# Kernel optimization log

Measured on AMD Instinct MI355X. Metric: run time of the kernel, lower is better.

The kernel has to match this reference:

```python
import jax, jax.numpy as jnp
import numpy as np

B, T, C = 8, 512, 512
H, HKV, D = 8, 4, 64
S_MAX = 128
BASE_FREQ = 10000.0
INIT_SIGMA = 256.0
EPS = 1e-6


def _init_positional_kernel(n_heads, head_dim, s_max, base_freq):
    table_size = 2 * s_max + 1
    deltas = jnp.arange(table_size) - s_max
    d_half = head_dim // 2
    freqs = 1.0 / base_freq ** (jnp.arange(d_half, dtype=jnp.float32) / d_half)
    phases = deltas[:, None].astype(jnp.float32) * freqs[None, :]
    P_single = jnp.concatenate([jnp.cos(phases), jnp.sin(phases)], axis=-1)
    return jnp.tile(P_single[None, :, :], (n_heads, 1, 1))


def setup_inputs() -> dict:
    key = jax.random.key(0)
    ks = jax.random.split(key, 6)
    scale = 0.02
    x = jax.random.normal(ks[0], (B, T, C), dtype=jnp.float32)
    Wq = jax.random.normal(ks[1], (C, H * D), dtype=jnp.float32) * scale
    Wk = jax.random.normal(ks[2], (C, HKV * D), dtype=jnp.float32) * scale
    Wv = jax.random.normal(ks[3], (C, HKV * D), dtype=jnp.float32) * scale
    Wproj = jax.random.normal(ks[4], (C, C), dtype=jnp.float32) * scale
    P = _init_positional_kernel(H, D, S_MAX, BASE_FREQ)
    sigma = jnp.full((H,), INIT_SIGMA, dtype=jnp.float32)
    return {"x": x, "Wq": Wq, "Wk": Wk, "Wv": Wv, "Wproj": Wproj, "P": P, "sigma": sigma}


def _norm(t):
    # nGPT-style: unit norm * sqrt(dim)
    dim = t.shape[-1]
    return t * (jnp.sqrt(float(dim)) * jax.lax.rsqrt((t * t).sum(axis=-1, keepdims=True) + EPS))


def _warped_kernel(P, sigma, T_):
    # P: [H, 2*S_MAX+1, D], sigma: [H] -> P_interp: [H, T, T, D]
    positions = jnp.arange(T_)
    delta = positions[:, None] - positions[None, :]  # [T, T]
    s = jnp.abs(sigma) + 1e-6
    delta_warped = S_MAX * jnp.tanh(delta[None, :, :].astype(jnp.float32) / s[:, None, None])
    delta_table = delta_warped + S_MAX  # [H, T, T]
    idx_lo = jnp.floor(delta_table).astype(jnp.int32)
    idx_hi = idx_lo + 1
    frac = delta_table - idx_lo.astype(P.dtype)
    table_max = 2 * S_MAX
    idx_lo = jnp.clip(idx_lo, 0, table_max)
    idx_hi = jnp.clip(idx_hi, 0, table_max)
    head_idx = jnp.arange(H)[:, None, None]
    P_lo = P[head_idx, idx_lo, :]  # [H, T, T, D]
    P_hi = P[head_idx, idx_hi, :]
    return (1 - frac[..., None]) * P_lo + frac[..., None] * P_hi


def reference(x, Wq, Wk, Wv, Wproj, P, sigma):
    q = (x @ Wq).reshape(B, T, H, D)
    k = (x @ Wk).reshape(B, T, HKV, D)
    v = (x @ Wv).reshape(B, T, HKV, D)
    q, k = _norm(q), _norm(k)
    repeats = H // HKV
    k = jnp.repeat(k, repeats, axis=2)
    v = jnp.repeat(v, repeats, axis=2)
    q = q.transpose(0, 2, 1, 3)  # [B, H, T, D]
    k = k.transpose(0, 2, 1, 3)
    v = v.transpose(0, 2, 1, 3)

    sm_scale = 1.0 / jnp.sqrt(float(D))
    P_interp = _warped_kernel(P, sigma, T)  # [H, T, T, D]
    S = jnp.einsum('bhid,hijd,bhjd->bhij', q, P_interp, k) * sm_scale
    causal_mask = jnp.tril(jnp.ones((T, T), dtype=jnp.bool_))
    S = jnp.where(causal_mask[None, None, :, :], S, jnp.finfo(S.dtype).min)
    A = jax.nn.softmax(S, axis=-1)
    y = A @ v  # [B, H, T, D]
    y = y.transpose(0, 2, 1, 3).reshape(B, T, H * D)
    return y @ Wproj
```

## Files before the change

kernel.cpp:

```cpp
#include <hip/hip_runtime.h>
#include <hip/hip_bf16.h>
#include <math.h>

#define Bb 8
#define Tt 512
#define Cc 512
#define Hh 8
#define HKV 4
#define Dd 64

typedef __attribute__((ext_vector_type(8))) short short8;
typedef __attribute__((ext_vector_type(4))) float float4v;
typedef __attribute__((ext_vector_type(2))) __fp16 h2;

__device__ __forceinline__ h2 u2h(unsigned u) {
  union { unsigned u; h2 h; } x; x.u = u; return x.h;
}
__device__ __forceinline__ unsigned h2u(h2 h) {
  union { h2 h; unsigned u; } x; x.h = h; return x.u;
}
__device__ __forceinline__ float fdot2(h2 a, h2 b, float c) {
#if __has_builtin(__builtin_amdgcn_fdot2)
  return __builtin_amdgcn_fdot2(a, b, c, false);
#else
  return fmaf((float)a.x, (float)b.x, fmaf((float)a.y, (float)b.y, c));
#endif
}

__device__ __forceinline__ float wave_reduce_sum(float v) {
#pragma unroll
  for (int off = 32; off > 0; off >>= 1) v += __shfl_xor(v, off, 64);
  return v;
}
__device__ __forceinline__ unsigned pack_bf2(float a, float b) {
  __hip_bfloat162 h = __float22bfloat162_rn(make_float2(a, b));
  return *(unsigned*)&h;
}

__global__ __launch_bounds__(256) void conv_x(const float* __restrict__ x,
                                              unsigned short* __restrict__ xb) {
  int i = (blockIdx.x * 256 + threadIdx.x) * 8;
  float4 f0 = *(const float4*)&x[i];
  float4 f1 = *(const float4*)&x[i + 4];
  unsigned u[4] = {pack_bf2(f0.x, f0.y), pack_bf2(f0.z, f0.w),
                   pack_bf2(f1.x, f1.y), pack_bf2(f1.z, f1.w)};
  *(uint4*)&xb[i] = *(uint4*)u;
}

__global__ __launch_bounds__(256) void conv_w(
    const float* __restrict__ Wq, const float* __restrict__ Wk,
    const float* __restrict__ Wv, const float* __restrict__ Wp,
    unsigned short* __restrict__ Wtq, unsigned short* __restrict__ Wtp) {
  __shared__ float Ts[64][65];
  const int k0 = blockIdx.x * 64;
  const int n0 = blockIdx.y * 64;
  const float* src; int ld, nc0; unsigned short* dst; int ndst;
  if (n0 < 512)       { src = Wq; ld = 512; nc0 = n0;        dst = Wtq; ndst = n0; }
  else if (n0 < 768)  { src = Wk; ld = 256; nc0 = n0 - 512;  dst = Wtq; ndst = n0; }
  else if (n0 < 1024) { src = Wv; ld = 256; nc0 = n0 - 768;  dst = Wtq; ndst = n0; }
  else                { src = Wp; ld = 512; nc0 = n0 - 1024; dst = Wtp; ndst = n0 - 1024; }
  const int t = threadIdx.x;
  const int r = t >> 4, c4 = (t & 15) << 2;
#pragma unroll
  for (int rr = 0; rr < 4; ++rr) {
    int row = (rr << 4) + r;
    float4 f = *(const float4*)&src[(k0 + row) * ld + nc0 + c4];
    Ts[row][c4] = f.x; Ts[row][c4 + 1] = f.y;
    Ts[row][c4 + 2] = f.z; Ts[row][c4 + 3] = f.w;
  }
  __syncthreads();
#pragma unroll
  for (int rr = 0; rr < 4; ++rr) {
    int nr = (rr << 4) + r;
    unsigned u0 = pack_bf2(Ts[c4][nr], Ts[c4 + 1][nr]);
    unsigned u1 = pack_bf2(Ts[c4 + 2][nr], Ts[c4 + 3][nr]);
    *(uint2*)&dst[(ndst + nr) * 512 + k0 + c4] = make_uint2(u0, u1);
  }
}

__global__ __launch_bounds__(256) void qkv_mfma(
    const unsigned short* __restrict__ xb, const unsigned short* __restrict__ Wt,
    unsigned short* __restrict__ qh, unsigned short* __restrict__ kh,
    unsigned* __restrict__ vhu) {
  __shared__ unsigned short As[64][64];
  __shared__ unsigned short Bs[64][64];
  const int m0 = blockIdx.x * 64;
  const int n0 = blockIdx.y * 64;
  const int t = threadIdx.x;
  const int w = t >> 6, lane = t & 63;
  const int srow = t >> 2, sc = (t & 3) << 4;
  float4v acc[4] = {{0,0,0,0},{0,0,0,0},{0,0,0,0},{0,0,0,0}};
  for (int k0 = 0; k0 < 512; k0 += 64) {
    uint4 a0 = *(const uint4*)&xb[(m0 + srow) * 512 + k0 + sc];
    uint4 a1 = *(const uint4*)&xb[(m0 + srow) * 512 + k0 + sc + 8];
    uint4 b0 = *(const uint4*)&Wt[(n0 + srow) * 512 + k0 + sc];
    uint4 b1 = *(const uint4*)&Wt[(n0 + srow) * 512 + k0 + sc + 8];
    __syncthreads();
    *(uint4*)&As[srow][sc] = a0; *(uint4*)&As[srow][sc + 8] = a1;
    *(uint4*)&Bs[srow][sc] = b0; *(uint4*)&Bs[srow][sc + 8] = b1;
    __syncthreads();
    const int ml = (w << 4) + (lane & 15);
    const int kq = (lane >> 4) << 3;
    short8 aF0 = *(short8*)&As[ml][kq];
    short8 aF1 = *(short8*)&As[ml][kq + 32];
#pragma unroll
    for (int nt = 0; nt < 4; ++nt) {
      const int nl = (nt << 4) + (lane & 15);
      short8 bF0 = *(short8*)&Bs[nl][kq];
      short8 bF1 = *(short8*)&Bs[nl][kq + 32];
      acc[nt] = __builtin_amdgcn_mfma_f32_16x16x32_bf16(aF0, bF0, acc[nt], 0, 0, 0);
      acc[nt] = __builtin_amdgcn_mfma_f32_16x16x32_bf16(aF1, bF1, acc[nt], 0, 0, 0);
    }
  }
  const int lane15 = lane & 15;
  const int rowbase = m0 + (w << 4) + ((lane >> 4) << 2);
  if (n0 < 768) {
#pragma unroll
    for (int r = 0; r < 4; ++r) {
      float ss = 0.0f;
#pragma unroll
      for (int nt = 0; nt < 4; ++nt) ss = fmaf(acc[nt][r], acc[nt][r], ss);
#pragma unroll
      for (int off = 1; off < 16; off <<= 1) ss += __shfl_xor(ss, off, 64);
      float sc2 = 8.0f * rsqrtf(ss + 1e-6f);
      const int row = rowbase + r;
      if (n0 < 512) {
        const int h = n0 >> 6;
#pragma unroll
        for (int nt = 0; nt < 4; ++nt) {
          __fp16 hv = (__fp16)(acc[nt][r] * sc2);
          qh[(row * Hh + h) * Dd + (nt << 4) + lane15] = *(unsigned short*)&hv;
        }
      } else {
        const int hkv = (n0 - 512) >> 6;
#pragma unroll
        for (int nt = 0; nt < 4; ++nt) {
          __fp16 hv = (__fp16)(acc[nt][r] * sc2);
          kh[(row * HKV + hkv) * Dd + (nt << 4) + lane15] = *(unsigned short*)&hv;
        }
      }
    }
  } else {
    const int hkv = (n0 - 768) >> 6;
#pragma unroll
    for (int r = 0; r < 4; r += 2) {
      const int rp = (rowbase + r) >> 1;
#pragma unroll
      for (int nt = 0; nt < 4; ++nt) {
        unsigned u = h2u(__builtin_amdgcn_cvt_pkrtz(acc[nt][r], acc[nt][r + 1]));
        vhu[(rp * HKV + hkv) * Dd + (nt << 4) + lane15] = u;
      }
    }
  }
}

__global__ __launch_bounds__(256) void proj_mfma(
    const unsigned short* __restrict__ yb, const unsigned short* __restrict__ Wt,
    float* __restrict__ out) {
  __shared__ unsigned short As[64][64];
  __shared__ unsigned short Bs[64][64];
  const int m0 = blockIdx.x * 64;
  const int n0 = blockIdx.y * 64;
  const int t = threadIdx.x;
  const int w = t >> 6, lane = t & 63;
  const int srow = t >> 2, sc = (t & 3) << 4;
  float4v acc[4] = {{0,0,0,0},{0,0,0,0},{0,0,0,0},{0,0,0,0}};
  for (int k0 = 0; k0 < 512; k0 += 64) {
    uint4 a0 = *(const uint4*)&yb[(m0 + srow) * 512 + k0 + sc];
    uint4 a1 = *(const uint4*)&yb[(m0 + srow) * 512 + k0 + sc + 8];
    uint4 b0 = *(const uint4*)&Wt[(n0 + srow) * 512 + k0 + sc];
    uint4 b1 = *(const uint4*)&Wt[(n0 + srow) * 512 + k0 + sc + 8];
    __syncthreads();
    *(uint4*)&As[srow][sc] = a0; *(uint4*)&As[srow][sc + 8] = a1;
    *(uint4*)&Bs[srow][sc] = b0; *(uint4*)&Bs[srow][sc + 8] = b1;
    __syncthreads();
    const int ml = (w << 4) + (lane & 15);
    const int kq = (lane >> 4) << 3;
    short8 aF0 = *(short8*)&As[ml][kq];
    short8 aF1 = *(short8*)&As[ml][kq + 32];
#pragma unroll
    for (int nt = 0; nt < 4; ++nt) {
      const int nl = (nt << 4) + (lane & 15);
      short8 bF0 = *(short8*)&Bs[nl][kq];
      short8 bF1 = *(short8*)&Bs[nl][kq + 32];
      acc[nt] = __builtin_amdgcn_mfma_f32_16x16x32_bf16(aF0, bF0, acc[nt], 0, 0, 0);
      acc[nt] = __builtin_amdgcn_mfma_f32_16x16x32_bf16(aF1, bF1, acc[nt], 0, 0, 0);
    }
  }
#pragma unroll
  for (int nt = 0; nt < 4; ++nt) {
    int col = n0 + (nt << 4) + (lane & 15);
#pragma unroll
    for (int r = 0; r < 4; ++r) {
      int row = m0 + (w << 4) + ((lane >> 4) << 2) + r;
      out[row * 512 + col] = acc[nt][r];
    }
  }
}

__global__ __launch_bounds__(256) void build_pw(const float* __restrict__ P,
                                                const float* __restrict__ sigma,
                                                unsigned short* __restrict__ Pwh) {
  int idx = blockIdx.x * blockDim.x + threadIdx.x;
  if (idx >= Hh * 1023 * 64) return;
  int d = idx & 63;
  int rem = idx >> 6;
  int dd = rem % 1023;
  int h = rem / 1023;
  float s = fabsf(sigma[h]) + 1e-6f;
  float delta = (float)(dd - 511);
  float dt = 128.0f * tanhf(delta / s) + 128.0f;
  float lo = floorf(dt);
  int ilo = (int)lo;
  float frac = dt - lo;
  ilo = max(0, min(ilo, 256));
  int ihi = min(ilo + 1, 256);
  const float* Pb = P + h * 257 * 64;
  float val = (1.0f - frac) * Pb[ilo * 64 + d] + frac * Pb[ihi * 64 + d];
  __fp16 hv = (__fp16)val;
  Pwh[idx] = *(unsigned short*)&hv;
}

__global__ __launch_bounds__(256) void attn(
    const unsigned short* __restrict__ qh, const unsigned short* __restrict__ kh,
    const unsigned* __restrict__ vhu, const unsigned short* __restrict__ Pwh,
    unsigned short* __restrict__ yb) {
  __shared__ __fp16 PwS[96][72];
  __shared__ __fp16 pS[4][32][16];

  const int t = threadIdx.x;
  const int lane = t & 63;
  const int wu = __builtin_amdgcn_readfirstlane(t >> 6);
  const int bh = blockIdx.x;
  const int b = bh >> 3;
  const int h = bh & 7;
  const int hkv = h >> 1;
  const int i0 = 480 - blockIdx.y * 32;

  float l_lane[8], o_run[8];
#pragma unroll
  for (int r = 0; r < 8; ++r) { l_lane[r] = 0.0f; o_run[r] = 0.0f; }

  const int prow = (wu << 3) + 63 - lane;
  const int i_base = i0 + (wu << 3);
  const unsigned short* qbase = &qh[((b * Tt + i_base) * Hh + h) * Dd];

  for (int jt0 = 0; jt0 <= i0 + 31; jt0 += 64) {
    __syncthreads();
    {
      int jr = t >> 2, dc = (t & 3) << 4;
      const int pb0 = h * 1023 + (i0 - jt0) + 448;
      const unsigned short* pwp = &Pwh[(pb0 + jr) * 64 + dc];
      *(uint4*)&PwS[jr][dc]     = *(const uint4*)&pwp[0];
      *(uint4*)&PwS[jr][dc + 8] = *(const uint4*)&pwp[8];
      int pr2 = 64 + (t >> 3), dc2 = (t & 7) << 3;
      if (pr2 < 95)
        *(uint4*)&PwS[pr2][dc2] = *(const uint4*)&Pwh[(pb0 + pr2) * 64 + dc2];
    }
    uint4 kr[8];
    {
      const uint4* kp = (const uint4*)&kh[((b * Tt + jt0 + lane) * HKV + hkv) * Dd];
#pragma unroll
      for (int c = 0; c < 8; ++c) kr[c] = kp[c];
    }
    __syncthreads();

    const int j = jt0 + lane;
    float pv8[8];
#pragma unroll
    for (int r = 0; r < 8; ++r) {
      const uint4* qp = (const uint4*)&qbase[r * (Hh * Dd)];
      float sr = 0.0f;
#pragma unroll
      for (int ch = 0; ch < 8; ++ch) {
        uint4 qu = qp[ch];
        uint4 pu = *(uint4*)&PwS[prow + r][ch << 3];
        sr = fdot2(u2h(qu.x) * u2h(pu.x), u2h(kr[ch].x), sr);
        sr = fdot2(u2h(qu.y) * u2h(pu.y), u2h(kr[ch].y), sr);
        sr = fdot2(u2h(qu.z) * u2h(pu.z), u2h(kr[ch].z), sr);
        sr = fdot2(u2h(qu.w) * u2h(pu.w), u2h(kr[ch].w), sr);
      }
      float sv = (j <= i_base + r) ? sr * 0.125f : -1e30f;
      float p = __expf(sv - 6.0f);
      l_lane[r] += p;
      pv8[r] = p;
    }
    {
      unsigned u[8];
#pragma unroll
      for (int r = 0; r < 8; ++r) {
        float other = __shfl_xor(pv8[r], 1, 64);
        u[r] = h2u(__builtin_amdgcn_cvt_pkrtz(pv8[r], other));
      }
      if (!(lane & 1)) {
        *(uint4*)&pS[wu][lane >> 1][0] = *(uint4*)&u[0];
        *(uint4*)&pS[wu][lane >> 1][8] = *(uint4*)&u[4];
      }
    }

    const unsigned* vp = &vhu[(((b * Tt + jt0) >> 1) * HKV + hkv) * Dd + lane];
#pragma unroll 4
    for (int j2 = 0; j2 < 32; ++j2) {
      uint4 p0 = *(uint4*)&pS[wu][j2][0];
      uint4 p1 = *(uint4*)&pS[wu][j2][8];
      h2 vv = u2h(vp[j2 * (HKV * Dd)]);
      o_run[0] = fdot2(u2h(p0.x), vv, o_run[0]);
      o_run[1] = fdot2(u2h(p0.y), vv, o_run[1]);
      o_run[2] = fdot2(u2h(p0.z), vv, o_run[2]);
      o_run[3] = fdot2(u2h(p0.w), vv, o_run[3]);
      o_run[4] = fdot2(u2h(p1.x), vv, o_run[4]);
      o_run[5] = fdot2(u2h(p1.y), vv, o_run[5]);
      o_run[6] = fdot2(u2h(p1.z), vv, o_run[6]);
      o_run[7] = fdot2(u2h(p1.w), vv, o_run[7]);
    }
  }
#pragma unroll
  for (int r = 0; r < 8; ++r) {
    float l = wave_reduce_sum(l_lane[r]);
    const int i_r = i_base + r;
    __hip_bfloat16 hv = __float2bfloat16(o_run[r] / l);
    yb[((b * Tt + i_r) * Hh + h) * Dd + lane] = *(unsigned short*)&hv;
  }
}

extern "C" void kernel_launch(void* const* d_in, const int* in_sizes, int n_in,
                              void* d_out, int out_size, void* d_ws, size_t ws_size,
                              hipStream_t stream) {
  const float* x     = (const float*)d_in[0];
  const float* Wq    = (const float*)d_in[1];
  const float* Wk    = (const float*)d_in[2];
  const float* Wv    = (const float*)d_in[3];
  const float* Wproj = (const float*)d_in[4];
  const float* P     = (const float*)d_in[5];
  const float* sigma = (const float*)d_in[6];
  float* out = (float*)d_out;

  float* ws = (float*)d_ws;
  unsigned short* qh  = (unsigned short*)ws;
  unsigned short* kh  = (unsigned short*)(ws + 1048576);
  unsigned*       vhu = (unsigned*)(ws + 1572864);
  unsigned short* Pwh = (unsigned short*)(ws + 2097152);
  unsigned short* xb  = (unsigned short*)(ws + 2359296);
  unsigned short* yb  = xb;
  unsigned short* Wtq = (unsigned short*)(ws + 3407872);
  unsigned short* Wtp = (unsigned short*)(ws + 3670016);

  conv_x<<<dim3(1024), 256, 0, stream>>>(x, xb);
  conv_w<<<dim3(8, 24), 256, 0, stream>>>(Wq, Wk, Wv, Wproj, Wtq, Wtp);
  qkv_mfma<<<dim3(64, 16), 256, 0, stream>>>(xb, Wtq, qh, kh, vhu);
  build_pw<<<dim3(2046), 256, 0, stream>>>(P, sigma, Pwh);
  attn<<<dim3(64, 16), 256, 0, stream>>>(qh, kh, vhu, Pwh, yb);
  proj_mfma<<<dim3(64, 8), 256, 0, stream>>>(yb, Wtp, out);
}
```

Measured before the change: 157.7 us.

## Enlarge QKV and projection GEMM tiles to 128x128 with 4x4 MFMA per wave

```diff
diff --git a/kernel.cpp b/kernel.cpp
--- a/kernel.cpp
+++ b/kernel.cpp
@@ -82,73 +82,100 @@
     const unsigned short* __restrict__ xb, const unsigned short* __restrict__ Wt,
     unsigned short* __restrict__ qh, unsigned short* __restrict__ kh,
     unsigned* __restrict__ vhu) {
-  __shared__ unsigned short As[64][64];
-  __shared__ unsigned short Bs[64][64];
-  const int m0 = blockIdx.x * 64;
-  const int n0 = blockIdx.y * 64;
+  __shared__ unsigned short As[128][64];
+  __shared__ unsigned short Bs[128][64];
+  const int m0 = blockIdx.x * 128;
+  const int n0 = blockIdx.y * 128;
   const int t = threadIdx.x;
   const int w = t >> 6, lane = t & 63;
-  const int srow = t >> 2, sc = (t & 3) << 4;
-  float4v acc[4] = {{0,0,0,0},{0,0,0,0},{0,0,0,0},{0,0,0,0}};
+  const int mw = (w >> 1) << 6;
+  const int nw = (w & 1) << 6;
+  const int srow = t >> 1, scol = (t & 1) << 5;
+  float4v acc[4][4];
+#pragma unroll
+  for (int mi = 0; mi < 4; ++mi)
+#pragma unroll
+    for (int ni = 0; ni < 4; ++ni) acc[mi][ni] = (float4v){0, 0, 0, 0};
+
   for (int k0 = 0; k0 < 512; k0 += 64) {
-    uint4 a0 = *(const uint4*)&xb[(m0 + srow) * 512 + k0 + sc];
-    uint4 a1 = *(const uint4*)&xb[(m0 + srow) * 512 + k0 + sc + 8];
-    uint4 b0 = *(const uint4*)&Wt[(n0 + srow) * 512 + k0 + sc];
-    uint4 b1 = *(const uint4*)&Wt[(n0 + srow) * 512 + k0 + sc + 8];
-    __syncthreads();
-    *(uint4*)&As[srow][sc] = a0; *(uint4*)&As[srow][sc + 8] = a1;
-    *(uint4*)&Bs[srow][sc] = b0; *(uint4*)&Bs[srow][sc + 8] = b1;
-    __syncthreads();
-    const int ml = (w << 4) + (lane & 15);
+    uint4 a[4], b[4];
+    const uint4* ap = (const uint4*)&xb[(m0 + srow) * 512 + k0 + scol];
+    const uint4* bp = (const uint4*)&Wt[(n0 + srow) * 512 + k0 + scol];
+#pragma unroll
+    for (int c = 0; c < 4; ++c) { a[c] = ap[c]; b[c] = bp[c]; }
+    __syncthreads();
+#pragma unroll
+    for (int c = 0; c < 4; ++c) {
+      ((uint4*)&As[srow][scol])[c] = a[c];
+      ((uint4*)&Bs[srow][scol])[c] = b[c];
+    }
+    __syncthreads();
+    const int lm = lane & 15;
     const int kq = (lane >> 4) << 3;
-    short8 aF0 = *(short8*)&As[ml][kq];
-    short8 aF1 = *(short8*)&As[ml][kq + 32];
-#pragma unroll
-    for (int nt = 0; nt < 4; ++nt) {
-      const int nl = (nt << 4) + (lane & 15);
-      short8 bF0 = *(short8*)&Bs[nl][kq];
-      short8 bF1 = *(short8*)&Bs[nl][kq + 32];
-      acc[nt] = __builtin_amdgcn_mfma_f32_16x16x32_bf16(aF0, bF0, acc[nt], 0, 0, 0);
-      acc[nt] = __builtin_amdgcn_mfma_f32_16x16x32_bf16(aF1, bF1, acc[nt], 0, 0, 0);
-    }
-  }
+#pragma unroll
+    for (int kh2 = 0; kh2 < 2; ++kh2) {
+      short8 aF[4], bF[4];
+#pragma unroll
+      for (int mi = 0; mi < 4; ++mi)
+        aF[mi] = *(short8*)&As[mw + mi * 16 + lm][kq + kh2 * 32];
+#pragma unroll
+      for (int ni = 0; ni < 4; ++ni)
+        bF[ni] = *(short8*)&Bs[nw + ni * 16 + lm][kq + kh2 * 32];
+#pragma unroll
+      for (int mi = 0; mi < 4; ++mi)
+#pragma unroll
+        for (int ni = 0; ni < 4; ++ni)
+          acc[mi][ni] = __builtin_amdgcn_mfma_f32_16x16x32_bf16(
+              aF[mi], bF[ni], acc[mi][ni], 0, 0, 0);
+    }
+  }
+
+  const int ncol = n0 + nw;
   const int lane15 = lane & 15;
-  const int rowbase = m0 + (w << 4) + ((lane >> 4) << 2);
-  if (n0 < 768) {
-#pragma unroll
-    for (int r = 0; r < 4; ++r) {
-      float ss = 0.0f;
-#pragma unroll
-      for (int nt = 0; nt < 4; ++nt) ss = fmaf(acc[nt][r], acc[nt][r], ss);
-#pragma unroll
-      for (int off = 1; off < 16; off <<= 1) ss += __shfl_xor(ss, off, 64);
-      float sc2 = 8.0f * rsqrtf(ss + 1e-6f);
-      const int row = rowbase + r;
-      if (n0 < 512) {
-        const int h = n0 >> 6;
-#pragma unroll
-        for (int nt = 0; nt < 4; ++nt) {
-          __fp16 hv = (__fp16)(acc[nt][r] * sc2);
-          qh[(row * Hh + h) * Dd + (nt << 4) + lane15] = *(unsigned short*)&hv;
-        }
-      } else {
-        const int hkv = (n0 - 512) >> 6;
-#pragma unroll
-        for (int nt = 0; nt < 4; ++nt) {
-          __fp16 hv = (__fp16)(acc[nt][r] * sc2);
-          kh[(row * HKV + hkv) * Dd + (nt << 4) + lane15] = *(unsigned short*)&hv;
+  if (ncol < 768) {
+#pragma unroll
+    for (int mi = 0; mi < 4; ++mi) {
+      const int rowb = m0 + mw + mi * 16 + ((lane >> 4) << 2);
+#pragma unroll
+      for (int r = 0; r < 4; ++r) {
+        float ss = 0.0f;
+#pragma unroll
+        for (int ni = 0; ni < 4; ++ni)
+          ss = fmaf(acc[mi][ni][r], acc[mi][ni][r], ss);
+#pragma unroll
+        for (int off = 1; off < 16; off <<= 1) ss += __shfl_xor(ss, off, 64);
+        float sc2 = 8.0f * rsqrtf(ss + 1e-6f);
+        const int row = rowb + r;
+        if (ncol < 512) {
+          const int h = ncol >> 6;
+#pragma unroll
+          for (int ni = 0; ni < 4; ++ni) {
+            __fp16 hv = (__fp16)(acc[mi][ni][r] * sc2);
+            qh[(row * Hh + h) * Dd + (ni << 4) + lane15] = *(unsigned short*)&hv;
+          }
+        } else {
+          const int hkv = (ncol - 512) >> 6;
+#pragma unroll
+          for (int ni = 0; ni < 4; ++ni) {
+            __fp16 hv = (__fp16)(acc[mi][ni][r] * sc2);
+            kh[(row * HKV + hkv) * Dd + (ni << 4) + lane15] = *(unsigned short*)&hv;
+          }
         }
       }
     }
   } else {
-    const int hkv = (n0 - 768) >> 6;
-#pragma unroll
-    for (int r = 0; r < 4; r += 2) {
-      const int rp = (rowbase + r) >> 1;
-#pragma unroll
-      for (int nt = 0; nt < 4; ++nt) {
-        unsigned u = h2u(__builtin_amdgcn_cvt_pkrtz(acc[nt][r], acc[nt][r + 1]));
-        vhu[(rp * HKV + hkv) * Dd + (nt << 4) + lane15] = u;
+    const int hkv = (ncol - 768) >> 6;
+#pragma unroll
+    for (int mi = 0; mi < 4; ++mi) {
+      const int rowb = m0 + mw + mi * 16 + ((lane >> 4) << 2);
+#pragma unroll
+      for (int r = 0; r < 4; r += 2) {
+        const int rp = (rowb + r) >> 1;
+#pragma unroll
+        for (int ni = 0; ni < 4; ++ni) {
+          unsigned u = h2u(__builtin_amdgcn_cvt_pkrtz(acc[mi][ni][r], acc[mi][ni][r + 1]));
+          vhu[(rp * HKV + hkv) * Dd + (ni << 4) + lane15] = u;
+        }
       }
     }
   }
@@ -157,43 +184,63 @@
 __global__ __launch_bounds__(256) void proj_mfma(
     const unsigned short* __restrict__ yb, const unsigned short* __restrict__ Wt,
     float* __restrict__ out) {
-  __shared__ unsigned short As[64][64];
-  __shared__ unsigned short Bs[64][64];
-  const int m0 = blockIdx.x * 64;
-  const int n0 = blockIdx.y * 64;
+  __shared__ unsigned short As[128][64];
+  __shared__ unsigned short Bs[128][64];
+  const int m0 = blockIdx.x * 128;
+  const int n0 = blockIdx.y * 128;
   const int t = threadIdx.x;
   const int w = t >> 6, lane = t & 63;
-  const int srow = t >> 2, sc = (t & 3) << 4;
-  float4v acc[4] = {{0,0,0,0},{0,0,0,0},{0,0,0,0},{0,0,0,0}};
+  const int mw = (w >> 1) << 6;
+  const int nw = (w & 1) << 6;
+  const int srow = t >> 1, scol = (t & 1) << 5;
+  float4v acc[4][4];
+#pragma unroll
+  for (int mi = 0; mi < 4; ++mi)
+#pragma unroll
+    for (int ni = 0; ni < 4; ++ni) acc[mi][ni] = (float4v){0, 0, 0, 0};
+
   for (int k0 = 0; k0 < 512; k0 += 64) {
-    uint4 a0 = *(const uint4*)&yb[(m0 + srow) * 512 + k0 + sc];
-    uint4 a1 = *(const uint4*)&yb[(m0 + srow) * 512 + k0 + sc + 8];
-    uint4 b0 = *(const uint4*)&Wt[(n0 + srow) * 512 + k0 + sc];
-    uint4 b1 = *(const uint4*)&Wt[(n0 + srow) * 512 + k0 + sc + 8];
-    __syncthreads();
-    *(uint4*)&As[srow][sc] = a0; *(uint4*)&As[srow][sc + 8] = a1;
-    *(uint4*)&Bs[srow][sc] = b0; *(uint4*)&Bs[srow][sc + 8] = b1;
-    __syncthreads();
-    const int ml = (w << 4) + (lane & 15);
+    uint4 a[4], b[4];
+    const uint4* ap = (const uint4*)&yb[(m0 + srow) * 512 + k0 + scol];
+    const uint4* bp = (const uint4*)&Wt[(n0 + srow) * 512 + k0 + scol];
+#pragma unroll
+    for (int c = 0; c < 4; ++c) { a[c] = ap[c]; b[c] = bp[c]; }
+    __syncthreads();
+#pragma unroll
+    for (int c = 0; c < 4; ++c) {
+      ((uint4*)&As[srow][scol])[c] = a[c];
+      ((uint4*)&Bs[srow][scol])[c] = b[c];
+    }
+    __syncthreads();
+    const int lm = lane & 15;
     const int kq = (lane >> 4) << 3;
-    short8 aF0 = *(short8*)&As[ml][kq];
-    short8 aF1 = *(short8*)&As[ml][kq + 32];
-#pragma unroll
-    for (int nt = 0; nt < 4; ++nt) {
-      const int nl = (nt << 4) + (lane & 15);
-      short8 bF0 = *(short8*)&Bs[nl][kq];
-      short8 bF1 = *(short8*)&Bs[nl][kq + 32];
-      acc[nt] = __builtin_amdgcn_mfma_f32_16x16x32_bf16(aF0, bF0, acc[nt], 0, 0, 0);
-      acc[nt] = __builtin_amdgcn_mfma_f32_16x16x32_bf16(aF1, bF1, acc[nt], 0, 0, 0);
-    }
-  }
-#pragma unroll
-  for (int nt = 0; nt < 4; ++nt) {
-    int col = n0 + (nt << 4) + (lane & 15);
-#pragma unroll
-    for (int r = 0; r < 4; ++r) {
-      int row = m0 + (w << 4) + ((lane >> 4) << 2) + r;
-      out[row * 512 + col] = acc[nt][r];
+#pragma unroll
+    for (int kh2 = 0; kh2 < 2; ++kh2) {
+      short8 aF[4], bF[4];
+#pragma unroll
+      for (int mi = 0; mi < 4; ++mi)
+        aF[mi] = *(short8*)&As[mw + mi * 16 + lm][kq + kh2 * 32];
+#pragma unroll
+      for (int ni = 0; ni < 4; ++ni)
+        bF[ni] = *(short8*)&Bs[nw + ni * 16 + lm][kq + kh2 * 32];
+#pragma unroll
+      for (int mi = 0; mi < 4; ++mi)
+#pragma unroll
+        for (int ni = 0; ni < 4; ++ni)
+          acc[mi][ni] = __builtin_amdgcn_mfma_f32_16x16x32_bf16(
+              aF[mi], bF[ni], acc[mi][ni], 0, 0, 0);
+    }
+  }
+  const int lane15 = lane & 15;
+#pragma unroll
+  for (int mi = 0; mi < 4; ++mi) {
+    const int rowb = m0 + mw + mi * 16 + ((lane >> 4) << 2);
+#pragma unroll
+    for (int ni = 0; ni < 4; ++ni) {
+      const int col = n0 + nw + (ni << 4) + lane15;
+#pragma unroll
+      for (int r = 0; r < 4; ++r)
+        out[(rowb + r) * 512 + col] = acc[mi][ni][r];
     }
   }
 }
@@ -347,8 +394,8 @@
 
   conv_x<<<dim3(1024), 256, 0, stream>>>(x, xb);
   conv_w<<<dim3(8, 24), 256, 0, stream>>>(Wq, Wk, Wv, Wproj, Wtq, Wtp);
-  qkv_mfma<<<dim3(64, 16), 256, 0, stream>>>(xb, Wtq, qh, kh, vhu);
+  qkv_mfma<<<dim3(32, 8), 256, 0, stream>>>(xb, Wtq, qh, kh, vhu);
   build_pw<<<dim3(2046), 256, 0, stream>>>(P, sigma, Pwh);
   attn<<<dim3(64, 16), 256, 0, stream>>>(qh, kh, vhu, Pwh, yb);
-  proj_mfma<<<dim3(64, 8), 256, 0, stream>>>(yb, Wtp, out);
-}
+  proj_mfma<<<dim3(32, 4), 256, 0, stream>>>(yb, Wtp, out);
+}
```

Measured after the change: 186.7 us. +18.4%, slower.
